# Performance work log

Measured on AMD Instinct MI355X. Metric: run time of the kernel, lower is better.

Reference implementation:

```python
import jax, jax.numpy as jnp
import numpy as np

B, C, D, S = 1024, 128, 16, 4        # nodes, channels (mul), irrep feature dim (0e+1o+2e+3o), species
K3, K2, K1 = 23, 5, 2                # generalized-CG path counts for correlation 3/2/1
OUT_DIMS = (1, 3)                    # target irreps 0e (dim 1) and 1o (dim 3)


def setup_inputs() -> dict:
    key = jax.random.key(0)
    ks = jax.random.split(key, 12)
    f = lambda k, s: jax.random.normal(k, s, dtype=jnp.float32)
    U_SCALE = 0.05  # keep corr-3 products numerically moderate (stand-in CG basis)
    return {
        "node_feats": f(ks[0], (B, C, D)),
        "u3_0": f(ks[1], (1, D, D, D, K3)) * U_SCALE,
        "u3_1": f(ks[2], (3, D, D, D, K3)) * U_SCALE,
        "u2_0": f(ks[3], (1, D, D, K2)) * U_SCALE,
        "u2_1": f(ks[4], (3, D, D, K2)) * U_SCALE,
        "u1_0": f(ks[5], (1, D, K1)) * U_SCALE,
        "u1_1": f(ks[6], (3, D, K1)) * U_SCALE,
        "w3": f(ks[7], (2, S, K3, C)) / np.sqrt(K3),
        "w2": f(ks[8], (2, S, K2, C)) / np.sqrt(K2),
        "w1": f(ks[9], (2, S, K1, C)) / np.sqrt(K1),
        "w_lin": f(ks[10], (2, C, C)),
        "node_species": jax.random.randint(ks[11], (B,), 0, S, dtype=jnp.int32),
    }


def _sym_contract(x, sp, u3, u2, u1, w3, w2, w1):
    """MACE symmetric contraction for one output irrep.
    x: (B,C,D); u3: (do,D,D,D,K3); u2: (do,D,D,K2); u1: (do,D,K1);
    w*: (S,K*,C) per-species path weights. Returns (B,C,do)."""
    onehot = jax.nn.one_hot(sp, S, dtype=x.dtype)        # (B,S)
    # corr-3 main term: fold species weights into the basis once (small: S*C*do*D^3)
    uw3 = jnp.einsum('oijlk,ekc->ecoijl', u3, w3)        # (S,C,do,D,D,D)
    do = u3.shape[0]
    out = jnp.zeros((x.shape[0], x.shape[1], do, D, D), x.dtype)
    for e in range(S):  # fixed small species loop (irregular per-species access)
        out = out + onehot[:, e][:, None, None, None, None] * \
            jnp.einsum('coijl,bcl->bcoij', uw3[e], x)
    # corr-2: add weighted basis, contract one feature axis
    c2 = jnp.einsum('oijk,bkc->bcoij', u2, w2[sp]) + out
    out = jnp.einsum('bcoij,bcj->bcoi', c2, x)
    # corr-1
    c1 = jnp.einsum('oik,bkc->bcoi', u1, w1[sp]) + out
    return jnp.einsum('bcoi,bci->bco', c1, x)            # (B,C,do)


def reference(node_feats, u3_0, u3_1, u2_0, u2_1, u1_0, u1_1, w3, w2, w1, w_lin, node_species):
    y0 = _sym_contract(node_feats, node_species, u3_0, u2_0, u1_0, w3[0], w2[0], w1[0])
    y1 = _sym_contract(node_feats, node_species, u3_1, u2_1, u1_1, w3[1], w2[1], w1[1])
    # equivariant Linear(target_irreps): mix multiplicity channels per irrep, 1/sqrt(fan_in)
    scale = 1.0 / jnp.sqrt(jnp.asarray(C, node_feats.dtype))
    z0 = jnp.einsum('bco,cn->bno', y0, w_lin[0]) * scale  # (B,C,1)
    z1 = jnp.einsum('bco,cn->bno', y1, w_lin[1]) * scale  # (B,C,3)
    # axis_to_mul flattening: (B, C*1 + C*3)
    return jnp.concatenate([z0.reshape(B, C * 1), z1.reshape(B, C * 3)], axis=1)
```

## Files before the change

kernel.cpp:

```cpp
#include <hip/hip_runtime.h>
#include <hip/hip_bf16.h>

#define SS 4
#define CC 128
#define WELEM 18432
#define NK3 23
#define NK2 5
#define NK1 2
#define DLP 72

typedef unsigned int uint;
typedef unsigned short ushort;
typedef __attribute__((ext_vector_type(8))) short bf16x8;
typedef __attribute__((ext_vector_type(4))) float f32x4;

__device__ __forceinline__ float bflo(uint u){ return __uint_as_float(u << 16); }
__device__ __forceinline__ float bfhi(uint u){ return __uint_as_float(u & 0xffff0000u); }
__device__ __forceinline__ ushort f2bf(float f) {
  uint u = __float_as_uint(f);
  return (ushort)((u + 0x7fffu + ((u >> 16) & 1u)) >> 16);
}
__device__ __forceinline__ uint pk2(float a, float b) {
  __hip_bfloat162 h = __float22bfloat162_rn(make_float2(a, b));
  return *(uint*)&h;
}

__global__ __launch_bounds__(256) void pre_kernel(
    const float* __restrict__ u3_0, const float* __restrict__ u3_1,
    const float* __restrict__ w3,
    const float* __restrict__ u2_0, const float* __restrict__ u2_1,
    const float* __restrict__ u1_0, const float* __restrict__ u1_1,
    const float* __restrict__ w2,  const float* __restrict__ w1,
    const int* __restrict__ sp, ushort* __restrict__ W,
    int* __restrict__ sorted, int* __restrict__ seg) {
  __shared__ float smem[5888 + NK3 * 64];
  int bx = blockIdx.x;
  int tid = threadIdx.x;

  if (bx < 512) {
    float* u3s = smem;
    float* w3s = smem + 5888;
    int ch = bx & 1, i = (bx >> 1) & 15, o = (bx >> 5) & 3, s = bx >> 7;
    int g = (o > 0) ? 1 : 0, og = g ? (o - 1) : 0;
    const float* u3 = g ? u3_1 : u3_0;

    const float4* u3p = (const float4*)(u3 + (size_t)(og * 16 + i) * 5888);
    for (int d = tid; d < 1472; d += 256) {
      float4 v = u3p[d];
      u3s[4 * d] = v.x; u3s[4 * d + 1] = v.y; u3s[4 * d + 2] = v.z; u3s[4 * d + 3] = v.w;
    }
    for (int t = tid; t < NK3 * 64; t += 256) {
      int k = t >> 6, cp = t & 63;
      w3s[t] = w3[((size_t)(g * SS + s) * NK3 + k) * CC + ch * 64 + cp];
    }
    __syncthreads();

    float acc[64];
    #pragma unroll
    for (int q = 0; q < 64; q++) acc[q] = 0.f;
    int jl = tid;
    for (int k = 0; k < NK3; k++) {
      float u3v = u3s[jl * NK3 + k];
      const float4* wp = (const float4*)&w3s[k * 64];
      #pragma unroll
      for (int cq = 0; cq < 16; cq++) {
        float4 wv = wp[cq];
        acc[cq * 4 + 0] = fmaf(u3v, wv.x, acc[cq * 4 + 0]);
        acc[cq * 4 + 1] = fmaf(u3v, wv.y, acc[cq * 4 + 1]);
        acc[cq * 4 + 2] = fmaf(u3v, wv.z, acc[cq * 4 + 2]);
        acc[cq * 4 + 3] = fmaf(u3v, wv.w, acc[cq * 4 + 3]);
      }
    }
    int n = o * 16 + i;
    #pragma unroll
    for (int cp = 0; cp < 64; cp++) {
      W[(size_t)(s * CC + ch * 64 + cp) * WELEM + n * 256 + jl] = f2bf(acc[cp]);
    }
  } else if (bx < 1024) {
    int b2 = bx - 512;
    int s = b2 >> 7, c = b2 & 127;
    int n = tid >> 2, lq = tid & 3;
    int o = n >> 4, i = n & 15;
    int g = (o > 0) ? 1 : 0, og = g ? (o - 1) : 0;
    const float* u2 = g ? u2_1 : u2_0;
    const float* u1 = g ? u1_1 : u1_0;

    float vals[8];
    #pragma unroll
    for (int t = 0; t < 8; t++) {
      int k = 256 + lq * 8 + t;
      float v = 0.f;
      if (k < 272) {
        int j = k - 256;
        #pragma unroll
        for (int k2 = 0; k2 < NK2; k2++)
          v = fmaf(u2[((size_t)(og * 16 + i) * 16 + j) * NK2 + k2],
                   w2[((size_t)(g * SS + s) * NK2 + k2) * CC + c], v);
      } else if (k == 272) {
        #pragma unroll
        for (int k2 = 0; k2 < NK1; k2++)
          v = fmaf(u1[(size_t)(og * 16 + i) * NK1 + k2],
                   w1[((size_t)(g * SS + s) * NK1 + k2) * CC + c], v);
      }
      vals[t] = v;
    }
    uint4 pk;
    pk.x = pk2(vals[0], vals[1]); pk.y = pk2(vals[2], vals[3]);
    pk.z = pk2(vals[4], vals[5]); pk.w = pk2(vals[6], vals[7]);
    size_t base = (size_t)(s * CC + c) * WELEM;
    size_t off = 16384 + ((size_t)o * 64 + lq * 16 + i) * 8;
    *(uint4*)(W + base + off) = pk;
  } else {
    __shared__ int cnt[SS];
    __shared__ int basep[SS + 1];
    if (tid < SS) cnt[tid] = 0;
    __syncthreads();
    int mysp[4], mypos[4];
    #pragma unroll
    for (int q = 0; q < 4; q++) {
      int node = q * 256 + tid;
      int s = sp[node];
      mysp[q] = s;
      mypos[q] = atomicAdd(&cnt[s], 1);
    }
    __syncthreads();
    if (tid == 0) {
      basep[0] = 0;
      for (int q = 0; q < SS; q++) basep[q + 1] = basep[q] + cnt[q];
      for (int q = 0; q <= SS; q++) seg[q] = basep[q];
    }
    __syncthreads();
    #pragma unroll
    for (int q = 0; q < 4; q++)
      sorted[basep[mysp[q]] + mypos[q]] = q * 256 + tid;
  }
}

__global__ __launch_bounds__(256, 2) void corr_kernel(
    const float* __restrict__ xg, const ushort* __restrict__ Wg,
    const int* __restrict__ sorted, const int* __restrict__ seg,
    float* __restrict__ y) {
  __shared__ uint4 Wl4[2304];
  __shared__ __align__(16) float xl[4][16][20];
  __shared__ __align__(16) ushort Dl[4 * 16 * DLP];
  int bx = blockIdx.x;
  int h = bx >> 9, s = (bx >> 7) & 3, c = bx & 127;
  int tid = threadIdx.x;
  int w = tid >> 6, lane = tid & 63;
  int lq = lane >> 4, ln = lane & 15;

  const uint4* wg = (const uint4*)(Wg + (size_t)(s * CC + c) * WELEM);

  for (int d = tid; d < 2048; d += 256) {
    int n = d >> 5, j = d & 31;
    int kt = j >> 2, lqj = j & 3;
    Wl4[(kt * 4 + (n >> 4)) * 64 + ((lqj * 16 + (n & 15)) ^ kt)] = wg[d];
  }
  Wl4[2048 + tid] = wg[2048 + tid];

  int s0 = seg[s], s1 = seg[s + 1];
  int nslab = (s1 - s0 + 63) >> 6;

  int svcur = 0;
  if (h < nslab) {
    int row = s0 + h * 64 + w * 16 + ln;
    svcur = sorted[min(row, s1 - 1)];
    float4 v = *((const float4*)(xg + ((size_t)svcur * CC + c) * 16) + lq);
    *(float4*)(&xl[w][ln][lq * 4]) = v;
  }
  __syncthreads();

  for (int kslab = h; kslab < nslab; kslab += 2) {
    float xv[16];
    #pragma unroll
    for (int q = 0; q < 4; q++) {
      float4 v = *(const float4*)(&xl[w][ln][q * 4]);
      xv[q * 4] = v.x; xv[q * 4 + 1] = v.y; xv[q * 4 + 2] = v.z; xv[q * 4 + 3] = v.w;
    }
    int svc = svcur;
    int rowc = s0 + kslab * 64 + w * 16 + ln;
    float4 xcn = make_float4(0.f, 0.f, 0.f, 0.f);
    int kn = kslab + 2;
    if (kn < nslab) {
      int row = s0 + kn * 64 + w * 16 + ln;
      svcur = sorted[min(row, s1 - 1)];
      xcn = *((const float4*)(xg + ((size_t)svcur * CC + c) * 16) + lq);
    }

    float xs8[8];
    #pragma unroll
    for (int t = 0; t < 8; t++) xs8[t] = (lq & 1) ? xv[8 + t] : xv[t];

    f32x4 acc[4];
    #pragma unroll
    for (int nt = 0; nt < 4; nt++) acc[nt] = (f32x4){0.f, 0.f, 0.f, 0.f};

    #pragma unroll
    for (int kt = 0; kt < 9; kt++) {
      uint4 av;
      if (kt < 8) {
        float xj = (lq & 2) ? xv[kt * 2 + 1] : xv[kt * 2];
        av.x = pk2(xj * xs8[0], xj * xs8[1]);
        av.y = pk2(xj * xs8[2], xj * xs8[3]);
        av.z = pk2(xj * xs8[4], xj * xs8[5]);
        av.w = pk2(xj * xs8[6], xj * xs8[7]);
      } else {
        av.x = pk2(xs8[0], xs8[1]);
        av.y = pk2(xs8[2], xs8[3]);
        av.z = pk2(xs8[4], xs8[5]);
        av.w = pk2(xs8[6], xs8[7]);
        if (lq == 2) av = make_uint4(0x3f80u, 0u, 0u, 0u);
        if (lq == 3) av = make_uint4(0u, 0u, 0u, 0u);
      }
      bf16x8 a = *(bf16x8*)&av;
      #pragma unroll
      for (int nt = 0; nt < 4; nt++) {
        uint4 bv;
        if (kt < 8) {
          bv = Wl4[(kt * 4 + nt) * 64 + (lane ^ kt)];
        } else {
          bv = Wl4[2048 + nt * 64 + lane];
        }
        bf16x8 b = *(bf16x8*)&bv;
        acc[nt] = __builtin_amdgcn_mfma_f32_16x16x32_bf16(a, b, acc[nt], 0, 0, 0);
      }
    }

    #pragma unroll
    for (int nt = 0; nt < 4; nt++)
      #pragma unroll
      for (int r = 0; r < 4; r++)
        Dl[(w * 16 + lq * 4 + r) * DLP + nt * 16 + ln] = f2bf(acc[nt][r]);
    const uint4* dp = (const uint4*)&Dl[(w * 16 + ln) * DLP + lq * 16];
    uint4 d0 = dp[0], d1 = dp[1];
    float r = 0.f;
    r = fmaf(bflo(d0.x), xv[0],  r); r = fmaf(bfhi(d0.x), xv[1],  r);
    r = fmaf(bflo(d0.y), xv[2],  r); r = fmaf(bfhi(d0.y), xv[3],  r);
    r = fmaf(bflo(d0.z), xv[4],  r); r = fmaf(bfhi(d0.z), xv[5],  r);
    r = fmaf(bflo(d0.w), xv[6],  r); r = fmaf(bfhi(d0.w), xv[7],  r);
    r = fmaf(bflo(d1.x), xv[8],  r); r = fmaf(bfhi(d1.x), xv[9],  r);
    r = fmaf(bflo(d1.y), xv[10], r); r = fmaf(bfhi(d1.y), xv[11], r);
    r = fmaf(bflo(d1.z), xv[12], r); r = fmaf(bfhi(d1.z), xv[13], r);
    r = fmaf(bflo(d1.w), xv[14], r); r = fmaf(bfhi(d1.w), xv[15], r);
    if (rowc < s1)
      y[((size_t)svc * CC + c) * 4 + lq] = r;

    if (kn < nslab)
      *(float4*)(&xl[w][ln][lq * 4]) = xcn;
  }
}

__global__ __launch_bounds__(128) void lin_kernel(
    const float* __restrict__ y, const float* __restrict__ w_lin,
    float* __restrict__ out) {
  int b = blockIdx.x;
  int n = threadIdx.x;
  const float4* yb4 = (const float4*)(y + (size_t)b * 512);
  float a0 = 0.f, a1 = 0.f, a2 = 0.f, a3 = 0.f;
  #pragma unroll 8
  for (int cc = 0; cc < CC; cc++) {
    float4 yv = yb4[cc];
    float wl0 = w_lin[(size_t)cc * CC + n];
    float wl1 = w_lin[16384 + (size_t)cc * CC + n];
    a0 = fmaf(yv.x, wl0, a0);
    a1 = fmaf(yv.y, wl1, a1);
    a2 = fmaf(yv.z, wl1, a2);
    a3 = fmaf(yv.w, wl1, a3);
  }
  const float scale = 0.08838834764831845f;
  out[(size_t)b * 512 + n] = a0 * scale;
  out[(size_t)b * 512 + 128 + (size_t)n * 3 + 0] = a1 * scale;
  out[(size_t)b * 512 + 128 + (size_t)n * 3 + 1] = a2 * scale;
  out[(size_t)b * 512 + 128 + (size_t)n * 3 + 2] = a3 * scale;
}

extern "C" void kernel_launch(void* const* d_in, const int* in_sizes, int n_in,
                              void* d_out, int out_size, void* d_ws, size_t ws_size,
                              hipStream_t stream) {
  const float* node_feats = (const float*)d_in[0];
  const float* u3_0 = (const float*)d_in[1];
  const float* u3_1 = (const float*)d_in[2];
  const float* u2_0 = (const float*)d_in[3];
  const float* u2_1 = (const float*)d_in[4];
  const float* u1_0 = (const float*)d_in[5];
  const float* u1_1 = (const float*)d_in[6];
  const float* w3   = (const float*)d_in[7];
  const float* w2   = (const float*)d_in[8];
  const float* w1   = (const float*)d_in[9];
  const float* wlin = (const float*)d_in[10];
  const int* species = (const int*)d_in[11];
  float* out = (float*)d_out;

  char* ws = (char*)d_ws;
  ushort* W  = (ushort*)ws;
  float* yb  = (float*)(ws + 18874368);
  int* sorted = (int*)(ws + 20971520);
  int* seg    = (int*)(ws + 20975616);

  pre_kernel<<<1025, 256, 0, stream>>>(u3_0, u3_1, w3, u2_0, u2_1, u1_0, u1_1,
                                       w2, w1, species, W, sorted, seg);
  corr_kernel<<<1024, 256, 0, stream>>>(node_feats, W, sorted, seg, yb);
  lin_kernel<<<1024, 128, 0, stream>>>(yb, wlin, out);
}
```

Measured before the change: 123.7 us.

## Process two node slabs per block to reuse staged weights, halving grid

The corr kernel now handles both 64-row slabs of a (species, channel) pair inside one block instead of splitting them across two blocks. Each block loads the per-channel weight tile into LDS once and applies it to two slabs, with the two MFMA chains interleaved for ILP, and prefetches the next pair. The aim is to halve the redundant global weight loads and LDS staging. In exchange the grid shrinks to 512 blocks, which lowers parallelism on a large GPU, and register pressure rises.

Measured after the change: 129.7 us. 4.8% more time.

```diff
diff --git a/kernel.cpp b/kernel.cpp
--- a/kernel.cpp
+++ b/kernel.cpp
@@ -141,10 +141,10 @@
     const int* __restrict__ sorted, const int* __restrict__ seg,
     float* __restrict__ y) {
   __shared__ uint4 Wl4[2304];
-  __shared__ __align__(16) float xl[4][16][20];
+  __shared__ __align__(16) float xl[2][4][16][20];
   __shared__ __align__(16) ushort Dl[4 * 16 * DLP];
   int bx = blockIdx.x;
-  int h = bx >> 9, s = (bx >> 7) & 3, c = bx & 127;
+  int s = bx >> 7, c = bx & 127;
   int tid = threadIdx.x;
   int w = tid >> 6, lane = tid & 63;
   int lq = lane >> 4, ln = lane & 15;
@@ -160,69 +160,91 @@
 
   int s0 = seg[s], s1 = seg[s + 1];
   int nslab = (s1 - s0 + 63) >> 6;
-
-  int svcur = 0;
-  if (h < nslab) {
-    int row = s0 + h * 64 + w * 16 + ln;
-    svcur = sorted[min(row, s1 - 1)];
-    float4 v = *((const float4*)(xg + ((size_t)svcur * CC + c) * 16) + lq);
-    *(float4*)(&xl[w][ln][lq * 4]) = v;
+  int npair = (nslab + 1) >> 1;
+
+  int sv0 = 0, sv1 = 0;
+  if (nslab > 0) {
+    int r0 = s0 + w * 16 + ln;
+    sv0 = sorted[min(r0, s1 - 1)];
+    float4 v0 = *((const float4*)(xg + ((size_t)sv0 * CC + c) * 16) + lq);
+    *(float4*)(&xl[0][w][ln][lq * 4]) = v0;
+    int r1 = s0 + 64 + w * 16 + ln;
+    sv1 = sorted[min(r1, s1 - 1)];
+    float4 v1 = *((const float4*)(xg + ((size_t)sv1 * CC + c) * 16) + lq);
+    *(float4*)(&xl[1][w][ln][lq * 4]) = v1;
   }
   __syncthreads();
 
-  for (int kslab = h; kslab < nslab; kslab += 2) {
-    float xv[16];
+  for (int t = 0; t < npair; t++) {
+    float xvA[16], xvB[16];
     #pragma unroll
     for (int q = 0; q < 4; q++) {
-      float4 v = *(const float4*)(&xl[w][ln][q * 4]);
-      xv[q * 4] = v.x; xv[q * 4 + 1] = v.y; xv[q * 4 + 2] = v.z; xv[q * 4 + 3] = v.w;
-    }
-    int svc = svcur;
-    int rowc = s0 + kslab * 64 + w * 16 + ln;
-    float4 xcn = make_float4(0.f, 0.f, 0.f, 0.f);
-    int kn = kslab + 2;
-    if (kn < nslab) {
-      int row = s0 + kn * 64 + w * 16 + ln;
-      svcur = sorted[min(row, s1 - 1)];
-      xcn = *((const float4*)(xg + ((size_t)svcur * CC + c) * 16) + lq);
-    }
-
-    float xs8[8];
-    #pragma unroll
-    for (int t = 0; t < 8; t++) xs8[t] = (lq & 1) ? xv[8 + t] : xv[t];
-
-    f32x4 acc[4];
-    #pragma unroll
-    for (int nt = 0; nt < 4; nt++) acc[nt] = (f32x4){0.f, 0.f, 0.f, 0.f};
+      float4 va = *(const float4*)(&xl[0][w][ln][q * 4]);
+      xvA[q * 4] = va.x; xvA[q * 4 + 1] = va.y; xvA[q * 4 + 2] = va.z; xvA[q * 4 + 3] = va.w;
+      float4 vb = *(const float4*)(&xl[1][w][ln][q * 4]);
+      xvB[q * 4] = vb.x; xvB[q * 4 + 1] = vb.y; xvB[q * 4 + 2] = vb.z; xvB[q * 4 + 3] = vb.w;
+    }
+    int svA = sv0, svB = sv1;
+    int rowA = s0 + (2 * t) * 64 + w * 16 + ln;
+    int rowB = rowA + 64;
+    float4 xc0 = make_float4(0.f, 0.f, 0.f, 0.f);
+    float4 xc1 = make_float4(0.f, 0.f, 0.f, 0.f);
+    bool pf = (t + 1 < npair);
+    if (pf) {
+      int r0 = s0 + (2 * t + 2) * 64 + w * 16 + ln;
+      sv0 = sorted[min(r0, s1 - 1)];
+      xc0 = *((const float4*)(xg + ((size_t)sv0 * CC + c) * 16) + lq);
+      int r1 = min(r0 + 64, s1 - 1);
+      sv1 = sorted[r1];
+      xc1 = *((const float4*)(xg + ((size_t)sv1 * CC + c) * 16) + lq);
+    }
+
+    float xs8A[8], xs8B[8];
+    #pragma unroll
+    for (int q = 0; q < 8; q++) {
+      xs8A[q] = (lq & 1) ? xvA[8 + q] : xvA[q];
+      xs8B[q] = (lq & 1) ? xvB[8 + q] : xvB[q];
+    }
+
+    f32x4 accA[4], accB[4];
+    #pragma unroll
+    for (int nt = 0; nt < 4; nt++) {
+      accA[nt] = (f32x4){0.f, 0.f, 0.f, 0.f};
+      accB[nt] = (f32x4){0.f, 0.f, 0.f, 0.f};
+    }
 
     #pragma unroll
     for (int kt = 0; kt < 9; kt++) {
-      uint4 av;
+      uint4 avA, avB;
       if (kt < 8) {
-        float xj = (lq & 2) ? xv[kt * 2 + 1] : xv[kt * 2];
-        av.x = pk2(xj * xs8[0], xj * xs8[1]);
-        av.y = pk2(xj * xs8[2], xj * xs8[3]);
-        av.z = pk2(xj * xs8[4], xj * xs8[5]);
-        av.w = pk2(xj * xs8[6], xj * xs8[7]);
+        float xjA = (lq & 2) ? xvA[kt * 2 + 1] : xvA[kt * 2];
+        avA.x = pk2(xjA * xs8A[0], xjA * xs8A[1]);
+        avA.y = pk2(xjA * xs8A[2], xjA * xs8A[3]);
+        avA.z = pk2(xjA * xs8A[4], xjA * xs8A[5]);
+        avA.w = pk2(xjA * xs8A[6], xjA * xs8A[7]);
+        float xjB = (lq & 2) ? xvB[kt * 2 + 1] : xvB[kt * 2];
+        avB.x = pk2(xjB * xs8B[0], xjB * xs8B[1]);
+        avB.y = pk2(xjB * xs8B[2], xjB * xs8B[3]);
+        avB.z = pk2(xjB * xs8B[4], xjB * xs8B[5]);
+        avB.w = pk2(xjB * xs8B[6], xjB * xs8B[7]);
       } else {
-        av.x = pk2(xs8[0], xs8[1]);
-        av.y = pk2(xs8[2], xs8[3]);
-        av.z = pk2(xs8[4], xs8[5]);
-        av.w = pk2(xs8[6], xs8[7]);
-        if (lq == 2) av = make_uint4(0x3f80u, 0u, 0u, 0u);
-        if (lq == 3) av = make_uint4(0u, 0u, 0u, 0u);
+        avA.x = pk2(xs8A[0], xs8A[1]); avA.y = pk2(xs8A[2], xs8A[3]);
+        avA.z = pk2(xs8A[4], xs8A[5]); avA.w = pk2(xs8A[6], xs8A[7]);
+        avB.x = pk2(xs8B[0], xs8B[1]); avB.y = pk2(xs8B[2], xs8B[3]);
+        avB.z = pk2(xs8B[4], xs8B[5]); avB.w = pk2(xs8B[6], xs8B[7]);
+        if (lq == 2) { avA = make_uint4(0x3f80u, 0u, 0u, 0u); avB = avA; }
+        if (lq == 3) { avA = make_uint4(0u, 0u, 0u, 0u); avB = avA; }
       }
-      bf16x8 a = *(bf16x8*)&av;
+      bf16x8 aA = *(bf16x8*)&avA;
+      bf16x8 aB = *(bf16x8*)&avB;
       #pragma unroll
       for (int nt = 0; nt < 4; nt++) {
         uint4 bv;
-        if (kt < 8) {
-          bv = Wl4[(kt * 4 + nt) * 64 + (lane ^ kt)];
-        } else {
-          bv = Wl4[2048 + nt * 64 + lane];
-        }
+        if (kt < 8) bv = Wl4[(kt * 4 + nt) * 64 + (lane ^ kt)];
+        else        bv = Wl4[2048 + nt * 64 + lane];
         bf16x8 b = *(bf16x8*)&bv;
-        acc[nt] = __builtin_amdgcn_mfma_f32_16x16x32_bf16(a, b, acc[nt], 0, 0, 0);
+        accA[nt] = __builtin_amdgcn_mfma_f32_16x16x32_bf16(aA, b, accA[nt], 0, 0, 0);
+        accB[nt] = __builtin_amdgcn_mfma_f32_16x16x32_bf16(aB, b, accB[nt], 0, 0, 0);
       }
     }
 
@@ -230,23 +252,47 @@
     for (int nt = 0; nt < 4; nt++)
       #pragma unroll
       for (int r = 0; r < 4; r++)
-        Dl[(w * 16 + lq * 4 + r) * DLP + nt * 16 + ln] = f2bf(acc[nt][r]);
-    const uint4* dp = (const uint4*)&Dl[(w * 16 + ln) * DLP + lq * 16];
-    uint4 d0 = dp[0], d1 = dp[1];
-    float r = 0.f;
-    r = fmaf(bflo(d0.x), xv[0],  r); r = fmaf(bfhi(d0.x), xv[1],  r);
-    r = fmaf(bflo(d0.y), xv[2],  r); r = fmaf(bfhi(d0.y), xv[3],  r);
-    r = fmaf(bflo(d0.z), xv[4],  r); r = fmaf(bfhi(d0.z), xv[5],  r);
-    r = fmaf(bflo(d0.w), xv[6],  r); r = fmaf(bfhi(d0.w), xv[7],  r);
-    r = fmaf(bflo(d1.x), xv[8],  r); r = fmaf(bfhi(d1.x), xv[9],  r);
-    r = fmaf(bflo(d1.y), xv[10], r); r = fmaf(bfhi(d1.y), xv[11], r);
-    r = fmaf(bflo(d1.z), xv[12], r); r = fmaf(bfhi(d1.z), xv[13], r);
-    r = fmaf(bflo(d1.w), xv[14], r); r = fmaf(bfhi(d1.w), xv[15], r);
-    if (rowc < s1)
-      y[((size_t)svc * CC + c) * 4 + lq] = r;
-
-    if (kn < nslab)
-      *(float4*)(&xl[w][ln][lq * 4]) = xcn;
+        Dl[(w * 16 + lq * 4 + r) * DLP + nt * 16 + ln] = f2bf(accA[nt][r]);
+    {
+      const uint4* dp = (const uint4*)&Dl[(w * 16 + ln) * DLP + lq * 16];
+      uint4 d0 = dp[0], d1 = dp[1];
+      float r = 0.f;
+      r = fmaf(bflo(d0.x), xvA[0],  r); r = fmaf(bfhi(d0.x), xvA[1],  r);
+      r = fmaf(bflo(d0.y), xvA[2],  r); r = fmaf(bfhi(d0.y), xvA[3],  r);
+      r = fmaf(bflo(d0.z), xvA[4],  r); r = fmaf(bfhi(d0.z), xvA[5],  r);
+      r = fmaf(bflo(d0.w), xvA[6],  r); r = fmaf(bfhi(d0.w), xvA[7],  r);
+      r = fmaf(bflo(d1.x), xvA[8],  r); r = fmaf(bfhi(d1.x), xvA[9],  r);
+      r = fmaf(bflo(d1.y), xvA[10], r); r = fmaf(bfhi(d1.y), xvA[11], r);
+      r = fmaf(bflo(d1.z), xvA[12], r); r = fmaf(bfhi(d1.z), xvA[13], r);
+      r = fmaf(bflo(d1.w), xvA[14], r); r = fmaf(bfhi(d1.w), xvA[15], r);
+      if (rowA < s1)
+        y[((size_t)svA * CC + c) * 4 + lq] = r;
+    }
+    #pragma unroll
+    for (int nt = 0; nt < 4; nt++)
+      #pragma unroll
+      for (int r = 0; r < 4; r++)
+        Dl[(w * 16 + lq * 4 + r) * DLP + nt * 16 + ln] = f2bf(accB[nt][r]);
+    {
+      const uint4* dp = (const uint4*)&Dl[(w * 16 + ln) * DLP + lq * 16];
+      uint4 d0 = dp[0], d1 = dp[1];
+      float r = 0.f;
+      r = fmaf(bflo(d0.x), xvB[0],  r); r = fmaf(bfhi(d0.x), xvB[1],  r);
+      r = fmaf(bflo(d0.y), xvB[2],  r); r = fmaf(bfhi(d0.y), xvB[3],  r);
+      r = fmaf(bflo(d0.z), xvB[4],  r); r = fmaf(bfhi(d0.z), xvB[5],  r);
+      r = fmaf(bflo(d0.w), xvB[6],  r); r = fmaf(bfhi(d0.w), xvB[7],  r);
+      r = fmaf(bflo(d1.x), xvB[8],  r); r = fmaf(bfhi(d1.x), xvB[9],  r);
+      r = fmaf(bflo(d1.y), xvB[10], r); r = fmaf(bfhi(d1.y), xvB[11], r);
+      r = fmaf(bflo(d1.z), xvB[12], r); r = fmaf(bfhi(d1.z), xvB[13], r);
+      r = fmaf(bflo(d1.w), xvB[14], r); r = fmaf(bfhi(d1.w), xvB[15], r);
+      if (rowB < s1)
+        y[((size_t)svB * CC + c) * 4 + lq] = r;
+    }
+
+    if (pf) {
+      *(float4*)(&xl[0][w][ln][lq * 4]) = xc0;
+      *(float4*)(&xl[1][w][ln][lq * 4]) = xc1;
+    }
   }
 }
 
@@ -299,6 +345,6 @@
 
   pre_kernel<<<1025, 256, 0, stream>>>(u3_0, u3_1, w3, u2_0, u2_1, u1_0, u1_1,
                                        w2, w1, species, W, sorted, seg);
-  corr_kernel<<<1024, 256, 0, stream>>>(node_feats, W, sorted, seg, yb);
+  corr_kernel<<<512, 256, 0, stream>>>(node_feats, W, sorted, seg, yb);
   lin_kernel<<<1024, 128, 0, stream>>>(yb, wlin, out);
 }
```
